# Performance work log

Hardware: AMD Instinct MI355X
Metric: run time of the kernel (lower is better)

Reference implementation:

```python
import jax, jax.numpy as jnp
import numpy as np

G, N_PER_G, V, H, DIN, DOUT, E = 1024, 64, 32, 128, 128, 10, 1048576
N = G * N_PER_G


def _lin(key, fan_in, fan_out):
    k1, k2 = jax.random.split(key)
    s = 1.0 / np.sqrt(fan_in)
    return (jax.random.uniform(k1, (fan_in, fan_out), jnp.float32, -s, s),
            jax.random.uniform(k2, (fan_out,), jnp.float32, -s, s))


def setup_inputs() -> dict:
    key = jax.random.key(0)
    ks = jax.random.split(key, 16)
    x = jax.random.normal(ks[0], (N, DIN), jnp.float32)
    # random edges constrained within each graph's contiguous node block
    gid = jax.random.randint(ks[1], (E,), 0, G)
    src = gid * N_PER_G + jax.random.randint(ks[2], (E,), 0, N_PER_G)
    dst = gid * N_PER_G + jax.random.randint(ks[3], (E,), 0, N_PER_G)
    edge_index = jnp.stack([src, dst]).astype(jnp.int64)
    batch = jnp.repeat(jnp.arange(G, dtype=jnp.int64), N_PER_G)
    edge_weights = jnp.ones((G, N_PER_G, V), jnp.float32) / V  # uniform init
    vemb = jax.random.normal(ks[4], (G, V, H), jnp.float32)
    vemb = vemb / jnp.linalg.norm(vemb, axis=-1, keepdims=True)
    W_emb, b_emb = _lin(ks[5], DIN, H)
    W_gcn, b_gcn = _lin(ks[6], H, H)
    aff_W1, aff_b1 = _lin(ks[7], H, H)
    aff_W2, aff_b2 = _lin(ks[8], H, H)
    vn_W1, vn_b1 = _lin(ks[9], H, H)
    vn_W2, vn_b2 = _lin(ks[10], H, H)
    mlp_W1, mlp_b1 = _lin(ks[11], H, H)
    mlp_W2, mlp_b2 = _lin(ks[12], H, DOUT)
    return dict(x=x, edge_index=edge_index, batch=batch, edge_weights=edge_weights,
                vemb=vemb, W_emb=W_emb, b_emb=b_emb, W_gcn=W_gcn, b_gcn=b_gcn,
                aff_W1=aff_W1, aff_b1=aff_b1, aff_W2=aff_W2, aff_b2=aff_b2,
                vn_W1=vn_W1, vn_b1=vn_b1, vn_W2=vn_W2, vn_b2=vn_b2,
                mlp_W1=mlp_W1, mlp_b1=mlp_b1, mlp_W2=mlp_W2, mlp_b2=mlp_b2)


def reference(x, edge_index, batch, edge_weights, vemb, W_emb, b_emb, W_gcn, b_gcn,
              aff_W1, aff_b1, aff_W2, aff_b2, vn_W1, vn_b1, vn_W2, vn_b2,
              mlp_W1, mlp_b1, mlp_W2, mlp_b2):
    n_nodes = x.shape[0]
    g, n, v = edge_weights.shape
    h = x @ W_emb + b_emb                                   # node embedding
    # GCNConv with self-loops and symmetric normalization
    hw = h @ W_gcn
    sl = jnp.arange(n_nodes)
    s = jnp.concatenate([edge_index[0], sl])
    d = jnp.concatenate([edge_index[1], sl])
    deg = jax.ops.segment_sum(jnp.ones_like(d, dtype=h.dtype), d, num_segments=n_nodes)
    inv = jax.lax.rsqrt(jnp.maximum(deg, 1.0))
    msg = hw[s] * (inv[s] * inv[d])[:, None]                # [E+N, H]
    h = jax.nn.relu(jax.ops.segment_sum(msg, d, num_segments=n_nodes) + b_gcn)
    # affinity MLP
    aff = jax.nn.relu(h @ aff_W1 + aff_b1) @ aff_W2 + aff_b2
    hg = h.reshape(g, n, -1)
    affg = aff.reshape(g, n, -1)
    # attention vs fixed normalized virtual-node embeddings
    att = jnp.einsum('gnh,gvh->gnv', affg, vemb) / jnp.sqrt(jnp.asarray(hg.shape[-1], h.dtype))
    ew = edge_weights * (1.0 + jax.nn.sigmoid(att))
    rs = ew.sum(axis=-1, keepdims=True)
    ew = ew / jnp.where(rs == 0, 1.0, rs)                   # row-normalize
    vn = jnp.einsum('gnv,gnh->gvh', ew, hg)                 # weighted scatter-pool
    vn = jax.nn.relu(vn @ vn_W1 + vn_b1) @ vn_W2 + vn_b2
    gf = vn.mean(axis=1)                                    # [G, H]
    return jax.nn.relu(gf @ mlp_W1 + mlp_b1) @ mlp_W2 + mlp_b2
```

## Files before the change

### kernel.cpp

```cpp
#include <hip/hip_runtime.h>
#include <hip/hip_bf16.h>
#include <cstddef>


#define EDGES 1048576
#define CAP 2048
#define SR 136
#define ST 72

typedef __attribute__((ext_vector_type(8))) short short8;
typedef __attribute__((ext_vector_type(4))) float f32x4;
typedef __hip_bfloat16 bf;
struct __align__(8) bf4 { bf v[4]; };

__global__ __launch_bounds__(256) void edge_hist(const int* __restrict__ ei,
                                                 unsigned* __restrict__ H)
{
    __shared__ unsigned lh[1024];
    int tid = threadIdx.x, b = blockIdx.x;
    for (int t = tid; t < 1024; t += 256) lh[t] = 0;
    __syncthreads();
    int base = b * 4096;
#pragma unroll 4
    for (int t = 0; t < 16; ++t) {
        int s = ei[base + t * 256 + tid];
        atomicAdd(&lh[s >> 6], 1u);
    }
    __syncthreads();
    for (int t = tid; t < 1024; t += 256) H[b * 1024 + t] = lh[t];
}

__global__ __launch_bounds__(256) void scan_conv(
    unsigned* __restrict__ H, unsigned* __restrict__ Tot,
    const float* __restrict__ w0, const float* __restrict__ w1,
    const float* __restrict__ w2, const float* __restrict__ w3,
    const float* __restrict__ w4, const float* __restrict__ w5,
    bf* __restrict__ outw)
{
    int b = blockIdx.x;
    if (b < 256) {
        int wv = threadIdx.x >> 6, lane = threadIdx.x & 63;
        int g = b * 4 + wv;
        unsigned v[4];
#pragma unroll
        for (int c = 0; c < 4; ++c) v[c] = H[(c * 64 + lane) * 1024 + g];
        unsigned run = 0;
#pragma unroll
        for (int c = 0; c < 4; ++c) {
            unsigned s = v[c];
            unsigned incl = s;
#pragma unroll
            for (int d = 1; d < 64; d <<= 1) {
                unsigned t = __shfl_up(incl, d);
                if (lane >= d) incl += t;
            }
            H[(c * 64 + lane) * 1024 + g] = run + (incl - s);
            run += __shfl(incl, 63);
        }
        if (lane == 0) Tot[g] = run;
    } else {
        int idx = (b - 256) * 256 + threadIdx.x;
        int n = idx >> 7, k = idx & 127;
        int off = (((n >> 4) * 4 + (k >> 5)) * 512) + (n & 15) * 32 + (k & 31);
        const float* srcs[6] = { w0, w1, w2, w3, w4, w5 };
#pragma unroll
        for (int m = 0; m < 6; ++m) {
            float vv = (m == 3) ? srcs[m][n * 128 + k] : srcs[m][k * 128 + n];
            outw[m * 16384 + off] = __float2bfloat16(vv);
        }
    }
}

__global__ __launch_bounds__(256) void edge_scatter(const int* __restrict__ ei,
                                                    const unsigned* __restrict__ H,
                                                    unsigned short* __restrict__ sorted)
{
    __shared__ unsigned lh[1024];
    __shared__ unsigned hrow[1024];
    int tid = threadIdx.x, b = blockIdx.x;
    for (int t = tid; t < 1024; t += 256) { lh[t] = 0; hrow[t] = H[b * 1024 + t]; }
    __syncthreads();
    int base = b * 4096;
    for (int t = 0; t < 16; ++t) {
        int e = base + t * 256 + tid;
        int s = ei[e], d = ei[EDGES + e];
        int g = s >> 6;
        unsigned r = atomicAdd(&lh[g], 1u);
        unsigned o = hrow[g] + r;
        if (o < (unsigned)CAP)
            sorted[(unsigned)g * CAP + o] = (unsigned short)(((d & 63) << 6) | (s & 63));
    }
}

__device__ __forceinline__ void loadB(const bf* __restrict__ gW, int wv, int l15,
                                      int kofs, short8* B)
{
#pragma unroll
    for (int ks = 0; ks < 4; ++ks)
        B[ks] = *(const short8*)(gW + (wv * 4 + ks) * 512 + l15 * 32 + kofs);
}

template<int MT, int KS, int SA>
__device__ __forceinline__ void mmaAB(const bf* sA, int rowA, int l15, int kofs,
                                      const short8* B, f32x4* acc)
{
#pragma unroll
    for (int ks = 0; ks < KS; ++ks) {
        short8 a[MT];
#pragma unroll
        for (int m = 0; m < MT; ++m)
            a[m] = *(const short8*)(sA + (rowA + m * 16 + l15) * SA + ks * 32 + kofs);
#pragma unroll
        for (int m = 0; m < MT; ++m)
            acc[m] = __builtin_amdgcn_mfma_f32_16x16x32_bf16(a[m], B[ks], acc[m], 0, 0, 0);
    }
}

template<int NT, int KS, int SB>
__device__ __forceinline__ void mmaBA(const bf* sB, int rowB, int l15, int kofs,
                                      const short8* A, f32x4* acc)
{
#pragma unroll
    for (int ks = 0; ks < KS; ++ks) {
        short8 b[NT];
#pragma unroll
        for (int nt = 0; nt < NT; ++nt)
            b[nt] = *(const short8*)(sB + (rowB + nt * 16 + l15) * SB + ks * 32 + kofs);
#pragma unroll
        for (int nt = 0; nt < NT; ++nt)
            acc[nt] = __builtin_amdgcn_mfma_f32_16x16x32_bf16(A[ks], b[nt], acc[nt], 0, 0, 0);
    }
}

template<int MT, int KS, int SA, int SB>
__device__ __forceinline__ void mmaABlds(const bf* sA, int rowA, const bf* sB, int rowB,
                                         int l15, int kofs, f32x4* acc)
{
#pragma unroll
    for (int ks = 0; ks < KS; ++ks) {
        short8 bb = *(const short8*)(sB + (rowB + l15) * SB + ks * 32 + kofs);
        short8 a[MT];
#pragma unroll
        for (int m = 0; m < MT; ++m)
            a[m] = *(const short8*)(sA + (rowA + m * 16 + l15) * SA + ks * 32 + kofs);
#pragma unroll
        for (int m = 0; m < MT; ++m)
            acc[m] = __builtin_amdgcn_mfma_f32_16x16x32_bf16(a[m], bb, acc[m], 0, 0, 0);
    }
}

__global__ __launch_bounds__(512, 2) void fused_graph(
    const float* __restrict__ x, const float* __restrict__ edge_w,
    const float* __restrict__ vemb, const bf* __restrict__ gWb,
    const float* __restrict__ b_emb,  const float* __restrict__ b_gcn,
    const float* __restrict__ aff_b1, const float* __restrict__ aff_b2,
    const float* __restrict__ vn_b1,  const float* __restrict__ vn_b2,
    const float* __restrict__ mlp_W1, const float* __restrict__ mlp_b1,
    const float* __restrict__ mlp_W2, const float* __restrict__ mlp_b2,
    const unsigned short* __restrict__ sorted,
    const unsigned* __restrict__ Tot,
    float* __restrict__ out)
{
    __shared__ __align__(16) bf sRM1[64 * SR];
    __shared__ __align__(16) bf sRM2[64 * SR];
    __shared__ __align__(16) bf sT1 [128 * ST];
    __shared__ __align__(16) bf sT2 [128 * ST];
    __shared__ __align__(16) bf sAdj[64 * ST];
    __shared__ float sInv[64];
    __shared__ float sBatt[32];

    unsigned* cnt = (unsigned*)sT1;
    bf* sVemb = sAdj;
    float* sPart = (float*)(sAdj + 4352);
    bf* sS    = sT1;
    bf* sEwnT = sT1 + 4608;
    float* sT2f = (float*)sT2;

    const int tid = threadIdx.x;
    const int g = blockIdx.x;
    const int wv = tid >> 6;
    const int lane = tid & 63;
    const int l15 = lane & 15;
    const int q = lane >> 4;
    const int kofs = q * 8;
    const int c = wv * 16 + l15;
    const int fq = wv * 16 + q * 4;

    short8 Bp[4], Bn[4];
    loadB(gWb, wv, l15, kofs, Bp);
    loadB(gWb + 16384, wv, l15, kofs, Bn);
    float4 xreg[4];
    const float4* gx = (const float4*)(x + (size_t)g * 8192);
#pragma unroll
    for (int t = 0; t < 4; ++t) xreg[t] = gx[tid + t * 512];
    float4 vreg[2];
    const float4* gv = (const float4*)(vemb + (size_t)g * 4096);
#pragma unroll
    for (int t = 0; t < 2; ++t) vreg[t] = gv[tid + t * 512];
    const int p6row = (wv & 3) * 16;
    const int p6v   = (wv >> 2) * 16 + l15;
    float ewreg[4];
#pragma unroll
    for (int r = 0; r < 4; ++r)
        ewreg[r] = edge_w[(size_t)g * 2048 + (p6row + q * 4 + r) * 32 + p6v];
    float bias_g = b_gcn[c], bias_v2 = vn_b2[c];
    unsigned ecnt = min(Tot[g], (unsigned)CAP);
    unsigned ebase = (unsigned)g * CAP;

#pragma unroll
    for (int t = 0; t < 2; ++t) cnt[tid * 2 + t] = 0u;
    __syncthreads();
    for (unsigned i = tid; i < ecnt; i += 512) {
        unsigned w = sorted[ebase + i];
        unsigned d = w >> 6, s = w & 63u;
        atomicAdd(&cnt[d * 16 + (s >> 2)], 1u << ((s & 3u) * 8));
    }
#pragma unroll
    for (int t = 0; t < 4; ++t) {
        int i = tid + t * 512;
        int row = i >> 5, c4 = i & 31;
        float4 w = xreg[t];
        bf4 tt;
        tt.v[0] = __float2bfloat16(w.x); tt.v[1] = __float2bfloat16(w.y);
        tt.v[2] = __float2bfloat16(w.z); tt.v[3] = __float2bfloat16(w.w);
        *(bf4*)(sRM1 + row * SR + c4 * 4) = tt;
    }
    __syncthreads();
    {
        int r = tid >> 3, q8 = tid & 7;
        float rs = 0.f;
#pragma unroll
        for (int t = 0; t < 2; ++t) {
            unsigned wd = cnt[r * 16 + q8 * 2 + t];
#pragma unroll
            for (int j = 0; j < 4; ++j) {
                int s = (q8 * 2 + t) * 4 + j;
                float v = (float)((wd >> (j * 8)) & 255u) + (s == r ? 1.f : 0.f);
                rs += v;
                sAdj[r * ST + s] = __float2bfloat16(v);
            }
        }
        rs += __shfl_xor(rs, 1);
        rs += __shfl_xor(rs, 2);
        rs += __shfl_xor(rs, 4);
        if (q8 == 0) sInv[r] = rsqrtf(rs);
    }
    __syncthreads();

    {
        f32x4 acc[4] = {};
        mmaBA<4, 4, SR>(sRM1, 0, l15, kofs, Bp, acc);
        loadB(gWb + 2 * 16384, wv, l15, kofs, Bp);
        f32x4 b4 = *(const f32x4*)(b_emb + fq);
#pragma unroll
        for (int nt = 0; nt < 4; ++nt) {
            bf4 tv;
#pragma unroll
            for (int r = 0; r < 4; ++r) tv.v[r] = __float2bfloat16(acc[nt][r] + b4[r]);
            *(bf4*)(sRM2 + (nt * 16 + l15) * SR + fq) = tv;
        }
    }
    __syncthreads();

    {
        f32x4 acc[4] = {};
        mmaAB<4, 4, SR>(sRM2, 0, l15, kofs, Bn, acc);
        loadB(gWb + 3 * 16384, wv, l15, kofs, Bn);
#pragma unroll
        for (int m = 0; m < 4; ++m) {
            bf4 tv;
#pragma unroll
            for (int r = 0; r < 4; ++r)
                tv.v[r] = __float2bfloat16(acc[m][r] * sInv[m * 16 + q * 4 + r]);
            *(bf4*)(sT1 + c * ST + m * 16 + q * 4) = tv;
        }
    }
    __syncthreads();

    {
        f32x4 acc[4] = {};
        mmaABlds<4, 2, ST, ST>(sAdj, 0, sT1, wv * 16, l15, kofs, acc);
#pragma unroll
        for (int m = 0; m < 4; ++m) {
            bf4 tv;
#pragma unroll
            for (int r = 0; r < 4; ++r) {
                float v = fmaxf(acc[m][r] * sInv[m * 16 + q * 4 + r] + bias_g, 0.f);
                sRM1[(m * 16 + q * 4 + r) * SR + c] = __float2bfloat16(v);
                tv.v[r] = __float2bfloat16(v);
            }
            *(bf4*)(sT2 + c * ST + m * 16 + q * 4) = tv;
        }
    }
    __syncthreads();

    {
#pragma unroll
        for (int t = 0; t < 2; ++t) {
            int i = tid + t * 512;
            int v = i >> 5, o4 = i & 31;
            float4 w = vreg[t];
            bf4 tt;
            tt.v[0] = __float2bfloat16(w.x); tt.v[1] = __float2bfloat16(w.y);
            tt.v[2] = __float2bfloat16(w.z); tt.v[3] = __float2bfloat16(w.w);
            *(bf4*)(sVemb + v * SR + o4 * 4) = tt;
        }
        f32x4 acc[4] = {};
        mmaBA<4, 4, SR>(sRM1, 0, l15, kofs, Bp, acc);
        loadB(gWb + 4 * 16384, wv, l15, kofs, Bp);
        f32x4 b4 = *(const f32x4*)(aff_b1 + fq);
#pragma unroll
        for (int nt = 0; nt < 4; ++nt) {
            bf4 tv;
#pragma unroll
            for (int r = 0; r < 4; ++r)
                tv.v[r] = __float2bfloat16(fmaxf(acc[nt][r] + b4[r], 0.f));
            *(bf4*)(sRM2 + (nt * 16 + l15) * SR + fq) = tv;
        }
    }
    __syncthreads();

    {
        f32x4 acc[2] = {};
        mmaBA<2, 4, SR>(sVemb, 0, l15, kofs, Bn, acc);
        loadB(gWb + 5 * 16384, wv, l15, kofs, Bn);
#pragma unroll
        for (int nt = 0; nt < 2; ++nt) {
            bf4 tv;
#pragma unroll
            for (int r = 0; r < 4; ++r) tv.v[r] = __float2bfloat16(acc[nt][r]);
            *(bf4*)(sS + (nt * 16 + l15) * SR + fq) = tv;
        }
        if (tid < 256) {
            int v = tid >> 3, sg = tid & 7;
            float s = 0.f;
            const bf* pv = sVemb + v * SR + sg * 16;
            const float* pb = aff_b2 + sg * 16;
#pragma unroll
            for (int o = 0; o < 16; ++o) s += pb[o] * __bfloat162float(pv[o]);
            s += __shfl_xor(s, 1); s += __shfl_xor(s, 2); s += __shfl_xor(s, 4);
            if (sg == 0) sBatt[v] = s;
        }
    }
    __syncthreads();

    {
        f32x4 acc = {};
        const int hv = wv >> 2;
#pragma unroll
        for (int ks = 0; ks < 4; ++ks) {
            short8 bb = *(const short8*)(sS + (hv * 16 + l15) * SR + ks * 32 + kofs);
            short8 a  = *(const short8*)(sRM2 + (p6row + l15) * SR + ks * 32 + kofs);
            acc = __builtin_amdgcn_mfma_f32_16x16x32_bf16(a, bb, acc, 0, 0, 0);
        }
        const float sc = 0.08838834764831845f;
        float bt = sBatt[p6v];
        float e[4];
#pragma unroll
        for (int r = 0; r < 4; ++r) {
            float att = (acc[r] + bt) * sc;
            e[r] = ewreg[r] * (1.f + 1.f / (1.f + __expf(-att)));
            float rs = e[r];
            rs += __shfl_xor(rs, 1); rs += __shfl_xor(rs, 2);
            rs += __shfl_xor(rs, 4); rs += __shfl_xor(rs, 8);
            if (l15 == 0) sPart[hv * 64 + p6row + q * 4 + r] = rs;
        }
        __syncthreads();
        bf4 tv;
#pragma unroll
        for (int r = 0; r < 4; ++r) {
            float rs = sPart[p6row + q * 4 + r] + sPart[64 + p6row + q * 4 + r];
            tv.v[r] = __float2bfloat16(e[r] / rs);
        }
        *(bf4*)(sEwnT + (hv * 16 + l15) * ST + p6row + q * 4) = tv;
    }
    __syncthreads();

    {
        f32x4 acc[2] = {};
#pragma unroll
        for (int ks = 0; ks < 2; ++ks) {
            short8 af = *(const short8*)(sT2 + (wv * 16 + l15) * ST + ks * 32 + kofs);
            short8 b0 = *(const short8*)(sEwnT + l15 * ST + ks * 32 + kofs);
            short8 b1 = *(const short8*)(sEwnT + (16 + l15) * ST + ks * 32 + kofs);
            acc[0] = __builtin_amdgcn_mfma_f32_16x16x32_bf16(af, b0, acc[0], 0, 0, 0);
            acc[1] = __builtin_amdgcn_mfma_f32_16x16x32_bf16(af, b1, acc[1], 0, 0, 0);
        }
#pragma unroll
        for (int nt = 0; nt < 2; ++nt) {
            bf4 tv;
#pragma unroll
            for (int r = 0; r < 4; ++r) tv.v[r] = __float2bfloat16(acc[nt][r]);
            *(bf4*)(sRM1 + (nt * 16 + l15) * SR + fq) = tv;
        }
    }
    __syncthreads();

    {
        f32x4 acc[2] = {};
        mmaBA<2, 4, SR>(sRM1, 0, l15, kofs, Bp, acc);
        f32x4 b4 = *(const f32x4*)(vn_b1 + fq);
#pragma unroll
        for (int nt = 0; nt < 2; ++nt) {
            bf4 tv;
#pragma unroll
            for (int r = 0; r < 4; ++r)
                tv.v[r] = __float2bfloat16(fmaxf(acc[nt][r] + b4[r], 0.f));
            *(bf4*)(sRM1 + (32 + nt * 16 + l15) * SR + fq) = tv;
        }
    }
    __syncthreads();

    {
        f32x4 acc[2] = {};
        mmaAB<2, 4, SR>(sRM1 + 32 * SR, 0, l15, kofs, Bn, acc);
#pragma unroll
        for (int m = 0; m < 2; ++m)
#pragma unroll
            for (int r = 0; r < 4; ++r)
                sT2f[c * 34 + m * 16 + q * 4 + r] = acc[m][r] + bias_v2;
    }
    __syncthreads();

    float* sF = (float*)sRM2;
    if (tid < 128) {
        float s = 0.f;
#pragma unroll
        for (int v = 0; v < 32; ++v) s += sT2f[tid * 34 + v];
        sF[tid] = s * 0.03125f;
    }
    __syncthreads();

    {
        int o = tid & 127, hh = tid >> 7;
        const float* w = mlp_W1 + (size_t)(hh * 32) * 128 + o;
        float a = 0.f;
#pragma unroll 8
        for (int k = 0; k < 32; ++k) a = fmaf(sF[hh * 32 + k], w[k * 128], a);
        sF[128 + hh * 128 + o] = a;
    }
    __syncthreads();
    if (tid < 128)
        sF[640 + tid] = fmaxf(sF[128 + tid] + sF[256 + tid] + sF[384 + tid]
                              + sF[512 + tid] + mlp_b1[tid], 0.f);
    __syncthreads();

    if (tid < 80) {
        int oo = tid >> 3, jg = tid & 7;
        float p = 0.f;
#pragma unroll
        for (int t2 = 0; t2 < 16; ++t2) {
            int j = jg * 16 + t2;
            p = fmaf(sF[640 + j], mlp_W2[j * 10 + oo], p);
        }
        p += __shfl_xor(p, 1); p += __shfl_xor(p, 2); p += __shfl_xor(p, 4);
        if (jg == 0) out[g * 10 + oo] = p + mlp_b2[oo];
    }
}

extern "C" void kernel_launch(void* const* d_in, const int* in_sizes, int n_in,
                              void* d_out, int out_size, void* d_ws, size_t ws_size,
                              hipStream_t stream)
{
    const float* x       = (const float*)d_in[0];
    const int*   ei      = (const int*)  d_in[1];
    const float* edge_w  = (const float*)d_in[3];
    const float* vemb    = (const float*)d_in[4];
    const float* W_emb   = (const float*)d_in[5];
    const float* b_emb   = (const float*)d_in[6];
    const float* W_gcn   = (const float*)d_in[7];
    const float* b_gcn   = (const float*)d_in[8];
    const float* aff_W1  = (const float*)d_in[9];
    const float* aff_b1  = (const float*)d_in[10];
    const float* aff_W2  = (const float*)d_in[11];
    const float* aff_b2  = (const float*)d_in[12];
    const float* vn_W1   = (const float*)d_in[13];
    const float* vn_b1   = (const float*)d_in[14];
    const float* vn_W2   = (const float*)d_in[15];
    const float* vn_b2   = (const float*)d_in[16];
    const float* mlp_W1  = (const float*)d_in[17];
    const float* mlp_b1  = (const float*)d_in[18];
    const float* mlp_W2  = (const float*)d_in[19];
    const float* mlp_b2  = (const float*)d_in[20];

    char* ws = (char*)d_ws;
    unsigned short* sorted = (unsigned short*)ws;
    unsigned* H    = (unsigned*)(ws + (4u << 20));
    unsigned* Tot  = (unsigned*)(ws + (5u << 20));
    bf*       gWb  = (bf*)      (ws + (5u << 20) + 65536);

    edge_hist  <<<dim3(256), dim3(256), 0, stream>>>(ei, H);
    scan_conv  <<<dim3(320), dim3(256), 0, stream>>>(
        H, Tot, W_emb, W_gcn, aff_W1, aff_W2, vn_W1, vn_W2, gWb);
    edge_scatter<<<dim3(256),dim3(256), 0, stream>>>(ei, H, sorted);
    fused_graph<<<dim3(1024), dim3(512), 0, stream>>>(
        x, edge_w, vemb, gWb, b_emb, b_gcn, aff_b1, aff_b2,
        vn_b1, vn_b2, mlp_W1, mlp_b1, mlp_W2, mlp_b2,
        sorted, Tot, (float*)d_out);
}
```

Measured before the change: 181.4 us.

## Commute mean before vn_W2 linear, fuse attention row-sum, drop barriers

Uses linearity to average the 32 virtual-node rows before applying vn_W2. This swaps a 32x128x128 MFMA for a 128x128 vector matvec read from global fp32 weights. The attention step now has each wave compute both 16-column halves, so the row sum is done by in-wave shuffles instead of a shared-memory partial exchange and an extra barrier. It also removes the barrier after the degree computation and folds the MLP partial sums into LDS atomics. Risks: the ReLU'd vn hidden state is averaged in bf16, and the removed barrier after the sInv write needs checking for correctness.

Result: slower. 185.6 us (+2.3%).

```diff
diff --git a/kernel.cpp b/kernel.cpp
--- a/kernel.cpp
+++ b/kernel.cpp
@@ -157,6 +157,7 @@
     const float* __restrict__ vn_b1,  const float* __restrict__ vn_b2,
     const float* __restrict__ mlp_W1, const float* __restrict__ mlp_b1,
     const float* __restrict__ mlp_W2, const float* __restrict__ mlp_b2,
+    const float* __restrict__ vn_W2,
     const unsigned short* __restrict__ sorted,
     const unsigned* __restrict__ Tot,
     float* __restrict__ out)
@@ -171,10 +172,9 @@
 
     unsigned* cnt = (unsigned*)sT1;
     bf* sVemb = sAdj;
-    float* sPart = (float*)(sAdj + 4352);
     bf* sS    = sT1;
     bf* sEwnT = sT1 + 4608;
-    float* sT2f = (float*)sT2;
+    float* sF = (float*)sRM2;
 
     const int tid = threadIdx.x;
     const int g = blockIdx.x;
@@ -198,12 +198,14 @@
 #pragma unroll
     for (int t = 0; t < 2; ++t) vreg[t] = gv[tid + t * 512];
     const int p6row = (wv & 3) * 16;
-    const int p6v   = (wv >> 2) * 16 + l15;
-    float ewreg[4];
-#pragma unroll
-    for (int r = 0; r < 4; ++r)
-        ewreg[r] = edge_w[(size_t)g * 2048 + (p6row + q * 4 + r) * 32 + p6v];
-    float bias_g = b_gcn[c], bias_v2 = vn_b2[c];
+    float ewreg[2][4];
+#pragma unroll
+    for (int nt = 0; nt < 2; ++nt)
+#pragma unroll
+        for (int r = 0; r < 4; ++r)
+            ewreg[nt][r] = edge_w[(size_t)g * 2048 + (p6row + q * 4 + r) * 32
+                                  + nt * 16 + l15];
+    float bias_g = b_gcn[c];
     unsigned ecnt = min(Tot[g], (unsigned)CAP);
     unsigned ebase = (unsigned)g * CAP;
 
@@ -226,6 +228,7 @@
         *(bf4*)(sRM1 + row * SR + c4 * 4) = tt;
     }
     __syncthreads();
+
     {
         int r = tid >> 3, q8 = tid & 7;
         float rs = 0.f;
@@ -245,8 +248,6 @@
         rs += __shfl_xor(rs, 4);
         if (q8 == 0) sInv[r] = rsqrtf(rs);
     }
-    __syncthreads();
-
     {
         f32x4 acc[4] = {};
         mmaBA<4, 4, SR>(sRM1, 0, l15, kofs, Bp, acc);
@@ -323,7 +324,6 @@
     {
         f32x4 acc[2] = {};
         mmaBA<2, 4, SR>(sVemb, 0, l15, kofs, Bn, acc);
-        loadB(gWb + 5 * 16384, wv, l15, kofs, Bn);
 #pragma unroll
         for (int nt = 0; nt < 2; ++nt) {
             bf4 tv;
@@ -345,34 +345,40 @@
     __syncthreads();
 
     {
-        f32x4 acc = {};
-        const int hv = wv >> 2;
+        f32x4 acc[2] = {};
 #pragma unroll
         for (int ks = 0; ks < 4; ++ks) {
-            short8 bb = *(const short8*)(sS + (hv * 16 + l15) * SR + ks * 32 + kofs);
             short8 a  = *(const short8*)(sRM2 + (p6row + l15) * SR + ks * 32 + kofs);
-            acc = __builtin_amdgcn_mfma_f32_16x16x32_bf16(a, bb, acc, 0, 0, 0);
+            short8 b0 = *(const short8*)(sS + l15 * SR + ks * 32 + kofs);
+            short8 b1 = *(const short8*)(sS + (16 + l15) * SR + ks * 32 + kofs);
+            acc[0] = __builtin_amdgcn_mfma_f32_16x16x32_bf16(a, b0, acc[0], 0, 0, 0);
+            acc[1] = __builtin_amdgcn_mfma_f32_16x16x32_bf16(a, b1, acc[1], 0, 0, 0);
         }
         const float sc = 0.08838834764831845f;
-        float bt = sBatt[p6v];
-        float e[4];
+        float bt[2] = { sBatt[l15], sBatt[16 + l15] };
+        float e[2][4];
 #pragma unroll
         for (int r = 0; r < 4; ++r) {
-            float att = (acc[r] + bt) * sc;
-            e[r] = ewreg[r] * (1.f + 1.f / (1.f + __expf(-att)));
-            float rs = e[r];
+#pragma unroll
+            for (int nt = 0; nt < 2; ++nt) {
+                float att = (acc[nt][r] + bt[nt]) * sc;
+                e[nt][r] = ewreg[nt][r] * (1.f + 1.f / (1.f + __expf(-att)));
+            }
+            float rs = e[0][r] + e[1][r];
             rs += __shfl_xor(rs, 1); rs += __shfl_xor(rs, 2);
             rs += __shfl_xor(rs, 4); rs += __shfl_xor(rs, 8);
-            if (l15 == 0) sPart[hv * 64 + p6row + q * 4 + r] = rs;
-        }
-        __syncthreads();
-        bf4 tv;
-#pragma unroll
-        for (int r = 0; r < 4; ++r) {
-            float rs = sPart[p6row + q * 4 + r] + sPart[64 + p6row + q * 4 + r];
-            tv.v[r] = __float2bfloat16(e[r] / rs);
-        }
-        *(bf4*)(sEwnT + (hv * 16 + l15) * ST + p6row + q * 4) = tv;
+            float ri = 1.f / rs;
+            e[0][r] *= ri; e[1][r] *= ri;
+        }
+        if (wv < 4) {
+#pragma unroll
+            for (int nt = 0; nt < 2; ++nt) {
+                bf4 tv;
+#pragma unroll
+                for (int r = 0; r < 4; ++r) tv.v[r] = __float2bfloat16(e[nt][r]);
+                *(bf4*)(sEwnT + (nt * 16 + l15) * ST + p6row + q * 4) = tv;
+            }
+        }
     }
     __syncthreads();
 
@@ -411,23 +417,26 @@
     }
     __syncthreads();
 
-    {
-        f32x4 acc[2] = {};
-        mmaAB<2, 4, SR>(sRM1 + 32 * SR, 0, l15, kofs, Bn, acc);
-#pragma unroll
-        for (int m = 0; m < 2; ++m)
-#pragma unroll
-            for (int r = 0; r < 4; ++r)
-                sT2f[c * 34 + m * 16 + q * 4 + r] = acc[m][r] + bias_v2;
-    }
-    __syncthreads();
-
-    float* sF = (float*)sRM2;
     if (tid < 128) {
         float s = 0.f;
 #pragma unroll
-        for (int v = 0; v < 32; ++v) s += sT2f[tid * 34 + v];
+        for (int v = 0; v < 32; ++v)
+            s += __bfloat162float(sRM1[(32 + v) * SR + tid]);
         sF[tid] = s * 0.03125f;
+    } else if (tid < 256) {
+        sF[tid] = vn_b2[tid - 128];
+    } else if (tid < 384) {
+        sF[tid] = mlp_b1[tid - 256];
+    }
+    __syncthreads();
+
+    {
+        int o = tid & 127, hh = tid >> 7;
+        const float* w = vn_W2 + (size_t)(hh * 32) * 128 + o;
+        float a = 0.f;
+#pragma unroll 8
+        for (int k = 0; k < 32; ++k) a = fmaf(sF[hh * 32 + k], w[k * 128], a);
+        atomicAdd(&sF[128 + o], a);
     }
     __syncthreads();
 
@@ -436,13 +445,9 @@
         const float* w = mlp_W1 + (size_t)(hh * 32) * 128 + o;
         float a = 0.f;
 #pragma unroll 8
-        for (int k = 0; k < 32; ++k) a = fmaf(sF[hh * 32 + k], w[k * 128], a);
-        sF[128 + hh * 128 + o] = a;
-    }
-    __syncthreads();
-    if (tid < 128)
-        sF[640 + tid] = fmaxf(sF[128 + tid] + sF[256 + tid] + sF[384 + tid]
-                              + sF[512 + tid] + mlp_b1[tid], 0.f);
+        for (int k = 0; k < 32; ++k) a = fmaf(sF[128 + hh * 32 + k], w[k * 128], a);
+        atomicAdd(&sF[256 + o], a);
+    }
     __syncthreads();
 
     if (tid < 80) {
@@ -451,7 +456,7 @@
 #pragma unroll
         for (int t2 = 0; t2 < 16; ++t2) {
             int j = jg * 16 + t2;
-            p = fmaf(sF[640 + j], mlp_W2[j * 10 + oo], p);
+            p = fmaf(fmaxf(sF[256 + j], 0.f), mlp_W2[j * 10 + oo], p);
         }
         p += __shfl_xor(p, 1); p += __shfl_xor(p, 2); p += __shfl_xor(p, 4);
         if (jg == 0) out[g * 10 + oo] = p + mlp_b2[oo];
@@ -495,6 +500,6 @@
     edge_scatter<<<dim3(256),dim3(256), 0, stream>>>(ei, H, sorted);
     fused_graph<<<dim3(1024), dim3(512), 0, stream>>>(
         x, edge_w, vemb, gWb, b_emb, b_gcn, aff_b1, aff_b2,
-        vn_b1, vn_b2, mlp_W1, mlp_b1, mlp_W2, mlp_b2,
+        vn_b1, vn_b2, mlp_W1, mlp_b1, mlp_W2, mlp_b2, vn_W2,
         sorted, Tot, (float*)d_out);
 }
```

## Retile dense GEMMs so each wave owns 32 features by half the rows

Applied to the files above, without the earlier changes.

The per-graph dense matmuls change their wave-to-tile mapping. Each of the 8 waves previously covered 16 output features across all 64 rows; now each covers 32 features across half the rows, holding twice as many weight fragments in registers. This halves the shared-memory activation reads per MFMA, since each A/B fragment feeds two MFMAs, at the cost of more VGPRs for the weight fragments. The vemb global load is also moved later, next to its use, to shorten register live ranges.

New measurement: 197.4 us. 8.8% more time.

```diff
diff --git a/kernel.cpp b/kernel.cpp
--- a/kernel.cpp
+++ b/kernel.cpp
@@ -92,43 +92,52 @@
     }
 }
 
-__device__ __forceinline__ void loadB(const bf* __restrict__ gW, int wv, int l15,
-                                      int kofs, short8* B)
-{
-#pragma unroll
-    for (int ks = 0; ks < 4; ++ks)
-        B[ks] = *(const short8*)(gW + (wv * 4 + ks) * 512 + l15 * 32 + kofs);
-}
-
-template<int MT, int KS, int SA>
-__device__ __forceinline__ void mmaAB(const bf* sA, int rowA, int l15, int kofs,
-                                      const short8* B, f32x4* acc)
-{
-#pragma unroll
-    for (int ks = 0; ks < KS; ++ks) {
+__device__ __forceinline__ void loadB2(const bf* __restrict__ gW, int fo, int l15,
+                                       int kofs, short8* B)
+{
+#pragma unroll
+    for (int f2 = 0; f2 < 2; ++f2)
+#pragma unroll
+        for (int ks = 0; ks < 4; ++ks)
+            B[f2 * 4 + ks] = *(const short8*)(gW + (((fo * 2 + f2) * 4 + ks) * 512)
+                                              + l15 * 32 + kofs);
+}
+
+template<int NT, int SB>
+__device__ __forceinline__ void mmaBA2(const bf* sB, int rowB, int l15, int kofs,
+                                       const short8* A, f32x4 (*acc)[NT])
+{
+#pragma unroll
+    for (int ks = 0; ks < 4; ++ks) {
+        short8 b[NT];
+#pragma unroll
+        for (int nt = 0; nt < NT; ++nt)
+            b[nt] = *(const short8*)(sB + (rowB + nt * 16 + l15) * SB + ks * 32 + kofs);
+#pragma unroll
+        for (int f2 = 0; f2 < 2; ++f2)
+#pragma unroll
+            for (int nt = 0; nt < NT; ++nt)
+                acc[f2][nt] = __builtin_amdgcn_mfma_f32_16x16x32_bf16(
+                    A[f2 * 4 + ks], b[nt], acc[f2][nt], 0, 0, 0);
+    }
+}
+
+template<int MT, int SA>
+__device__ __forceinline__ void mmaAB2(const bf* sA, int rowA, int l15, int kofs,
+                                       const short8* B, f32x4 (*acc)[2])
+{
+#pragma unroll
+    for (int ks = 0; ks < 4; ++ks) {
         short8 a[MT];
 #pragma unroll
         for (int m = 0; m < MT; ++m)
             a[m] = *(const short8*)(sA + (rowA + m * 16 + l15) * SA + ks * 32 + kofs);
 #pragma unroll
         for (int m = 0; m < MT; ++m)
-            acc[m] = __builtin_amdgcn_mfma_f32_16x16x32_bf16(a[m], B[ks], acc[m], 0, 0, 0);
-    }
-}
-
-template<int NT, int KS, int SB>
-__device__ __forceinline__ void mmaBA(const bf* sB, int rowB, int l15, int kofs,
-                                      const short8* A, f32x4* acc)
-{
-#pragma unroll
-    for (int ks = 0; ks < KS; ++ks) {
-        short8 b[NT];
-#pragma unroll
-        for (int nt = 0; nt < NT; ++nt)
-            b[nt] = *(const short8*)(sB + (rowB + nt * 16 + l15) * SB + ks * 32 + kofs);
-#pragma unroll
-        for (int nt = 0; nt < NT; ++nt)
-            acc[nt] = __builtin_amdgcn_mfma_f32_16x16x32_bf16(A[ks], b[nt], acc[nt], 0, 0, 0);
+#pragma unroll
+            for (int f2 = 0; f2 < 2; ++f2)
+                acc[m][f2] = __builtin_amdgcn_mfma_f32_16x16x32_bf16(
+                    a[m], B[f2 * 4 + ks], acc[m][f2], 0, 0, 0);
     }
 }
 
@@ -185,25 +194,24 @@
     const int kofs = q * 8;
     const int c = wv * 16 + l15;
     const int fq = wv * 16 + q * 4;
-
-    short8 Bp[4], Bn[4];
-    loadB(gWb, wv, l15, kofs, Bp);
-    loadB(gWb + 16384, wv, l15, kofs, Bn);
+    const int fo = wv & 3;
+    const int nh = wv >> 2;
+    const int fb = fo * 32;
+
+    short8 Bp[8], Bn[8];
+    loadB2(gWb, fo, l15, kofs, Bp);
+    loadB2(gWb + 16384, fo, l15, kofs, Bn);
     float4 xreg[4];
     const float4* gx = (const float4*)(x + (size_t)g * 8192);
 #pragma unroll
     for (int t = 0; t < 4; ++t) xreg[t] = gx[tid + t * 512];
-    float4 vreg[2];
-    const float4* gv = (const float4*)(vemb + (size_t)g * 4096);
-#pragma unroll
-    for (int t = 0; t < 2; ++t) vreg[t] = gv[tid + t * 512];
-    const int p6row = (wv & 3) * 16;
-    const int p6v   = (wv >> 2) * 16 + l15;
+    const int p6row = fo * 16;
+    const int p6v   = nh * 16 + l15;
     float ewreg[4];
 #pragma unroll
     for (int r = 0; r < 4; ++r)
         ewreg[r] = edge_w[(size_t)g * 2048 + (p6row + q * 4 + r) * 32 + p6v];
-    float bias_g = b_gcn[c], bias_v2 = vn_b2[c];
+    float bias_g = b_gcn[c];
     unsigned ecnt = min(Tot[g], (unsigned)CAP);
     unsigned ebase = (unsigned)g * CAP;
 
@@ -248,31 +256,39 @@
     __syncthreads();
 
     {
-        f32x4 acc[4] = {};
-        mmaBA<4, 4, SR>(sRM1, 0, l15, kofs, Bp, acc);
-        loadB(gWb + 2 * 16384, wv, l15, kofs, Bp);
-        f32x4 b4 = *(const f32x4*)(b_emb + fq);
-#pragma unroll
-        for (int nt = 0; nt < 4; ++nt) {
-            bf4 tv;
-#pragma unroll
-            for (int r = 0; r < 4; ++r) tv.v[r] = __float2bfloat16(acc[nt][r] + b4[r]);
-            *(bf4*)(sRM2 + (nt * 16 + l15) * SR + fq) = tv;
-        }
-    }
-    __syncthreads();
-
-    {
-        f32x4 acc[4] = {};
-        mmaAB<4, 4, SR>(sRM2, 0, l15, kofs, Bn, acc);
-        loadB(gWb + 3 * 16384, wv, l15, kofs, Bn);
-#pragma unroll
-        for (int m = 0; m < 4; ++m) {
-            bf4 tv;
-#pragma unroll
-            for (int r = 0; r < 4; ++r)
-                tv.v[r] = __float2bfloat16(acc[m][r] * sInv[m * 16 + q * 4 + r]);
-            *(bf4*)(sT1 + c * ST + m * 16 + q * 4) = tv;
+        f32x4 acc[2][2] = {};
+        mmaBA2<2, SR>(sRM1, nh * 32, l15, kofs, Bp, acc);
+        loadB2(gWb + 2 * 16384, fo, l15, kofs, Bp);
+#pragma unroll
+        for (int f2 = 0; f2 < 2; ++f2) {
+            f32x4 b4 = *(const f32x4*)(b_emb + fb + f2 * 16 + q * 4);
+#pragma unroll
+            for (int nt = 0; nt < 2; ++nt) {
+                bf4 tv;
+#pragma unroll
+                for (int r = 0; r < 4; ++r)
+                    tv.v[r] = __float2bfloat16(acc[f2][nt][r] + b4[r]);
+                *(bf4*)(sRM2 + (nh * 32 + nt * 16 + l15) * SR + fb + f2 * 16 + q * 4) = tv;
+            }
+        }
+    }
+    __syncthreads();
+
+    {
+        f32x4 acc[2][2] = {};
+        mmaAB2<2, SR>(sRM2, nh * 32, l15, kofs, Bn, acc);
+        loadB2(gWb + 3 * 16384, fo, l15, kofs, Bn);
+#pragma unroll
+        for (int m = 0; m < 2; ++m) {
+            f32x4 iv = *(const f32x4*)(sInv + nh * 32 + m * 16 + q * 4);
+#pragma unroll
+            for (int f2 = 0; f2 < 2; ++f2) {
+                bf4 tv;
+#pragma unroll
+                for (int r = 0; r < 4; ++r)
+                    tv.v[r] = __float2bfloat16(acc[m][f2][r] * iv[r]);
+                *(bf4*)(sT1 + (fb + f2 * 16 + l15) * ST + nh * 32 + m * 16 + q * 4) = tv;
+            }
         }
     }
     __syncthreads();
@@ -295,6 +311,13 @@
     __syncthreads();
 
     {
+        float4 vreg[2];
+        const float4* gv = (const float4*)(vemb + (size_t)g * 4096);
+#pragma unroll
+        for (int t = 0; t < 2; ++t) vreg[t] = gv[tid + t * 512];
+        f32x4 acc[2][2] = {};
+        mmaBA2<2, SR>(sRM1, nh * 32, l15, kofs, Bp, acc);
+        loadB2(gWb + 4 * 16384, fo, l15, kofs, Bp);
 #pragma unroll
         for (int t = 0; t < 2; ++t) {
             int i = tid + t * 512;
@@ -305,31 +328,31 @@
             tt.v[2] = __float2bfloat16(w.z); tt.v[3] = __float2bfloat16(w.w);
             *(bf4*)(sVemb + v * SR + o4 * 4) = tt;
         }
-        f32x4 acc[4] = {};
-        mmaBA<4, 4, SR>(sRM1, 0, l15, kofs, Bp, acc);
-        loadB(gWb + 4 * 16384, wv, l15, kofs, Bp);
-        f32x4 b4 = *(const f32x4*)(aff_b1 + fq);
-#pragma unroll
-        for (int nt = 0; nt < 4; ++nt) {
+#pragma unroll
+        for (int f2 = 0; f2 < 2; ++f2) {
+            f32x4 b4 = *(const f32x4*)(aff_b1 + fb + f2 * 16 + q * 4);
+#pragma unroll
+            for (int nt = 0; nt < 2; ++nt) {
+                bf4 tv;
+#pragma unroll
+                for (int r = 0; r < 4; ++r)
+                    tv.v[r] = __float2bfloat16(fmaxf(acc[f2][nt][r] + b4[r], 0.f));
+                *(bf4*)(sRM2 + (nh * 32 + nt * 16 + l15) * SR + fb + f2 * 16 + q * 4) = tv;
+            }
+        }
+    }
+    __syncthreads();
+
+    {
+        f32x4 acc[2][1] = {};
+        mmaBA2<1, SR>(sVemb, nh * 16, l15, kofs, Bn, acc);
+        loadB2(gWb + 5 * 16384, fo, l15, kofs, Bn);
+#pragma unroll
+        for (int f2 = 0; f2 < 2; ++f2) {
             bf4 tv;
 #pragma unroll
-            for (int r = 0; r < 4; ++r)
-                tv.v[r] = __float2bfloat16(fmaxf(acc[nt][r] + b4[r], 0.f));
-            *(bf4*)(sRM2 + (nt * 16 + l15) * SR + fq) = tv;
-        }
-    }
-    __syncthreads();
-
-    {
-        f32x4 acc[2] = {};
-        mmaBA<2, 4, SR>(sVemb, 0, l15, kofs, Bn, acc);
-        loadB(gWb + 5 * 16384, wv, l15, kofs, Bn);
-#pragma unroll
-        for (int nt = 0; nt < 2; ++nt) {
-            bf4 tv;
-#pragma unroll
-            for (int r = 0; r < 4; ++r) tv.v[r] = __float2bfloat16(acc[nt][r]);
-            *(bf4*)(sS + (nt * 16 + l15) * SR + fq) = tv;
+            for (int r = 0; r < 4; ++r) tv.v[r] = __float2bfloat16(acc[f2][0][r]);
+            *(bf4*)(sS + (nh * 16 + l15) * SR + fb + f2 * 16 + q * 4) = tv;
         }
         if (tid < 256) {
             int v = tid >> 3, sg = tid & 7;
@@ -346,10 +369,9 @@
 
     {
         f32x4 acc = {};
-        const int hv = wv >> 2;
 #pragma unroll
         for (int ks = 0; ks < 4; ++ks) {
-            short8 bb = *(const short8*)(sS + (hv * 16 + l15) * SR + ks * 32 + kofs);
+            short8 bb = *(const short8*)(sS + (nh * 16 + l15) * SR + ks * 32 + kofs);
             short8 a  = *(const short8*)(sRM2 + (p6row + l15) * SR + ks * 32 + kofs);
             acc = __builtin_amdgcn_mfma_f32_16x16x32_bf16(a, bb, acc, 0, 0, 0);
         }
@@ -363,7 +385,7 @@
             float rs = e[r];
             rs += __shfl_xor(rs, 1); rs += __shfl_xor(rs, 2);
             rs += __shfl_xor(rs, 4); rs += __shfl_xor(rs, 8);
-            if (l15 == 0) sPart[hv * 64 + p6row + q * 4 + r] = rs;
+            if (l15 == 0) sPart[nh * 64 + p6row + q * 4 + r] = rs;
         }
         __syncthreads();
         bf4 tv;
@@ -372,7 +394,7 @@
             float rs = sPart[p6row + q * 4 + r] + sPart[64 + p6row + q * 4 + r];
             tv.v[r] = __float2bfloat16(e[r] / rs);
         }
-        *(bf4*)(sEwnT + (hv * 16 + l15) * ST + p6row + q * 4) = tv;
+        *(bf4*)(sEwnT + (nh * 16 + l15) * ST + p6row + q * 4) = tv;
     }
     __syncthreads();
 
@@ -397,28 +419,31 @@
     __syncthreads();
 
     {
-        f32x4 acc[2] = {};
-        mmaBA<2, 4, SR>(sRM1, 0, l15, kofs, Bp, acc);
-        f32x4 b4 = *(const f32x4*)(vn_b1 + fq);
-#pragma unroll
-        for (int nt = 0; nt < 2; ++nt) {
+        f32x4 acc[2][1] = {};
+        mmaBA2<1, SR>(sRM1, nh * 16, l15, kofs, Bp, acc);
+#pragma unroll
+        for (int f2 = 0; f2 < 2; ++f2) {
+            f32x4 b4 = *(const f32x4*)(vn_b1 + fb + f2 * 16 + q * 4);
             bf4 tv;
 #pragma unroll
             for (int r = 0; r < 4; ++r)
-                tv.v[r] = __float2bfloat16(fmaxf(acc[nt][r] + b4[r], 0.f));
-            *(bf4*)(sRM1 + (32 + nt * 16 + l15) * SR + fq) = tv;
-        }
-    }
-    __syncthreads();
-
-    {
-        f32x4 acc[2] = {};
-        mmaAB<2, 4, SR>(sRM1 + 32 * SR, 0, l15, kofs, Bn, acc);
-#pragma unroll
-        for (int m = 0; m < 2; ++m)
+                tv.v[r] = __float2bfloat16(fmaxf(acc[f2][0][r] + b4[r], 0.f));
+            *(bf4*)(sRM1 + (32 + nh * 16 + l15) * SR + fb + f2 * 16 + q * 4) = tv;
+        }
+    }
+    __syncthreads();
+
+    {
+        f32x4 acc[1][2] = {};
+        mmaAB2<1, SR>(sRM1 + 32 * SR, nh * 16, l15, kofs, Bn, acc);
+#pragma unroll
+        for (int f2 = 0; f2 < 2; ++f2) {
+            float bv2 = vn_b2[fb + f2 * 16 + l15];
 #pragma unroll
             for (int r = 0; r < 4; ++r)
-                sT2f[c * 34 + m * 16 + q * 4 + r] = acc[m][r] + bias_v2;
+                sT2f[(fb + f2 * 16 + l15) * 34 + nh * 16 + q * 4 + r] =
+                    acc[0][f2][r] + bv2;
+        }
     }
     __syncthreads();
 
```
